# Kernel tuning notes

Hardware: AMD Instinct MI355X
Metric: run time of the kernel (lower is better)

Reference implementation:

```python
import jax, jax.numpy as jnp
import numpy as np

N_INST = 131072      # total patches across all bags
D_EMB = 512          # VGG16 pooling='max' output dim
ATT_UNITS = 128
CLS_UNITS = 512
NUM_BAGS = 256


def setup_inputs() -> dict:
    key = jax.random.key(0)
    ks = jax.random.split(key, 16)
    first_emb = jax.random.normal(ks[0], (N_INST, D_EMB), dtype=jnp.float32)
    first_lab = jnp.sort(jax.random.randint(ks[1], (N_INST,), 0, NUM_BAGS)).astype(jnp.int64)
    s = 0.02
    return {
        "first_emb": first_emb,
        "first_lab": first_lab,
        # first-level attention head: Dense(tanh) -> Dense(1, sigmoid)
        "W_a1": jax.random.normal(ks[2], (D_EMB, ATT_UNITS), dtype=jnp.float32) * s,
        "b_a1": jnp.zeros((ATT_UNITS,), dtype=jnp.float32),
        "w_o1": jax.random.normal(ks[3], (ATT_UNITS, 1), dtype=jnp.float32) * s,
        "b_o1": jnp.zeros((1,), dtype=jnp.float32),
        # second-level attention head
        "W_a2": jax.random.normal(ks[4], (D_EMB, ATT_UNITS), dtype=jnp.float32) * s,
        "b_a2": jnp.zeros((ATT_UNITS,), dtype=jnp.float32),
        "w_o2": jax.random.normal(ks[5], (ATT_UNITS, 1), dtype=jnp.float32) * s,
        "b_o2": jnp.zeros((1,), dtype=jnp.float32),
        # classifier: Dense(CLS_UNITS, linear) -> Dense(1, sigmoid)
        "W_c": jax.random.normal(ks[6], (D_EMB, CLS_UNITS), dtype=jnp.float32) * s,
        "b_c": jnp.zeros((CLS_UNITS,), dtype=jnp.float32),
        "w_out": jax.random.normal(ks[7], (CLS_UNITS, 1), dtype=jnp.float32) * s,
        "b_out": jnp.zeros((1,), dtype=jnp.float32),
    }


def reference(first_emb, first_lab, W_a1, b_a1, w_o1, b_o1,
              W_a2, b_a2, w_o2, b_o2, W_c, b_c, w_out, b_out):
    # --- first-level (instance) attention ---
    a1 = jnp.tanh(first_emb @ W_a1 + b_a1)                 # [N, A]
    att1 = jax.nn.sigmoid(a1 @ w_o1 + b_o1)                # [N, 1]
    # tf: transpose(softmax(transpose(att))) == softmax over the N axis (global)
    fst_att = jax.nn.softmax(att1, axis=0)                 # [N, 1]
    # --- per-bag attention-weighted sum (fused segment reduce) ---
    # replaces the python loop of gather_nd + matmul over contiguous bags
    second_emb = jax.ops.segment_sum(fst_att * first_emb, first_lab,
                                     num_segments=NUM_BAGS)  # [B, D]
    # --- second-level (bag) attention ---
    a2 = jnp.tanh(second_emb @ W_a2 + b_a2)                # [B, A]
    att2 = jax.nn.sigmoid(a2 @ w_o2 + b_o2)                # [B, 1]
    snd_att = jax.nn.softmax(att2.T, axis=-1)              # [1, B]
    outer_bag_emb = snd_att @ second_emb                   # [1, D]
    # --- classifier (dropout is identity at inference) ---
    h = outer_bag_emb @ W_c + b_c                          # [1, CLS]
    pred = jax.nn.sigmoid(h @ w_out + b_out)               # [1, 1]
    return pred
```

## Files before the change

### kernel.cpp

```cpp
#include <hip/hip_runtime.h>
#include <cstdint>
#include <cstddef>

#define N_INST 131072
#define D_EMB  512
#define ATT    128
#define NBAGS  256
#define TILE_I 32
#define LDA    520
#define NBLK   512
#define NTILES (N_INST / TILE_I)
#define TPB    (NTILES / NBLK)
#define NZ1    32

typedef __attribute__((ext_vector_type(8))) short  bf16x8;
typedef __attribute__((ext_vector_type(4))) float  f32x4;
typedef __attribute__((ext_vector_type(4))) unsigned short u16x4;


__device__ inline unsigned short f2b(float f) {
    unsigned u = __builtin_bit_cast(unsigned, f);
    u += 0x7FFFu + ((u >> 16) & 1u);
    return (unsigned short)(u >> 16);
}

__device__ inline float fast_tanh(float x) {
    float e = __expf(2.f * x);
    return 1.f - 2.f / (e + 1.f);
}

__global__ __launch_bounds__(256) void k_prep_wt(
    const float* __restrict__ Wa1, unsigned short* __restrict__ Wt)
{
    const int n = blockIdx.x;
    for (int k = threadIdx.x; k < D_EMB; k += 256)
        Wt[(size_t)n * D_EMB + k] = f2b(Wa1[(size_t)k * ATT + n]);
}

__global__ __launch_bounds__(256, 2) void k_att1(
    const float* __restrict__ emb, const int* __restrict__ lab,
    const unsigned short* __restrict__ Wt, const float* __restrict__ ba1,
    const float* __restrict__ wo1, const float* __restrict__ bo1,
    float* __restrict__ rawr, int R, float* __restrict__ Z1s)
{
    __shared__ unsigned short Ash[2][TILE_I * LDA];
    __shared__ float att4[4][TILE_I];
    __shared__ float sval[TILE_I];
    __shared__ int   labs[2][TILE_I];

    const int t  = threadIdx.x;
    const int w  = t >> 6;
    const int l  = t & 63;
    const int l4 = l & 15;
    const int h4 = l >> 4;
    const int n0 = 16 * (2 * w) + l4;
    const int n1 = 16 * (2 * w + 1) + l4;
    const size_t tile0 = (size_t)blockIdx.x * TPB;
    float* __restrict__ raw = rawr + (size_t)(blockIdx.x % R) * (NBAGS * D_EMB);

    const float ba1v0 = ba1[n0], ba1v1 = ba1[n1];
    const float wo1v0 = wo1[n0], wo1v1 = wo1[n1];

    {
        const size_t i0 = tile0 * TILE_I;
        float4 v[16];
        #pragma unroll
        for (int j = 0; j < 16; ++j) {
            int idx = j * 256 + t;
            int row = idx >> 7;
            int c4  = (idx & 127) * 4;
            v[j] = *reinterpret_cast<const float4*>(&emb[(i0 + row) * D_EMB + c4]);
        }
        if (t < TILE_I) labs[0][t] = lab[i0 + t];
        #pragma unroll
        for (int j = 0; j < 16; ++j) {
            int idx = j * 256 + t;
            int row = idx >> 7;
            int c4  = (idx & 127) * 4;
            u16x4 b = { f2b(v[j].x), f2b(v[j].y), f2b(v[j].z), f2b(v[j].w) };
            *reinterpret_cast<u16x4*>(&Ash[0][row * LDA + c4]) = b;
        }
    }
    __syncthreads();

    int   cur_bag = -1;
    float ar0 = 0.f, ar1 = 0.f;
    float z1acc = 0.f;
    int   p = 0;

    for (int it = 0; it < TPB; ++it) {
        const bool hasNext = (it + 1 < TPB);
        const size_t i0n = (tile0 + it + 1) * TILE_I;

        float4 v[16];
        int nlab = 0;
        if (hasNext) {
            #pragma unroll
            for (int j = 0; j < 16; ++j) {
                int idx = j * 256 + t;
                int row = idx >> 7;
                int c4  = (idx & 127) * 4;
                v[j] = *reinterpret_cast<const float4*>(
                    &emb[(i0n + row) * D_EMB + c4]);
            }
            if (t < TILE_I) nlab = lab[i0n + t];
        }

        f32x4 acc00 = {0.f,0.f,0.f,0.f}, acc01 = {0.f,0.f,0.f,0.f};
        f32x4 acc10 = {0.f,0.f,0.f,0.f}, acc11 = {0.f,0.f,0.f,0.f};
        #pragma unroll
        for (int ks = 0; ks < 16; ++ks) {
            bf16x8 b0 = *reinterpret_cast<const bf16x8*>(
                &Wt[(size_t)n0 * D_EMB + 32 * ks + 8 * h4]);
            bf16x8 b1 = *reinterpret_cast<const bf16x8*>(
                &Wt[(size_t)n1 * D_EMB + 32 * ks + 8 * h4]);
            bf16x8 a0 = *reinterpret_cast<const bf16x8*>(
                &Ash[p][(l4) * LDA + 32 * ks + 8 * h4]);
            bf16x8 a1 = *reinterpret_cast<const bf16x8*>(
                &Ash[p][(16 + l4) * LDA + 32 * ks + 8 * h4]);
            acc00 = __builtin_amdgcn_mfma_f32_16x16x32_bf16(a0, b0, acc00, 0, 0, 0);
            acc01 = __builtin_amdgcn_mfma_f32_16x16x32_bf16(a0, b1, acc01, 0, 0, 0);
            acc10 = __builtin_amdgcn_mfma_f32_16x16x32_bf16(a1, b0, acc10, 0, 0, 0);
            acc11 = __builtin_amdgcn_mfma_f32_16x16x32_bf16(a1, b1, acc11, 0, 0, 0);
        }

        #pragma unroll
        for (int rt = 0; rt < 2; ++rt) {
            #pragma unroll
            for (int reg = 0; reg < 4; ++reg) {
                float pp = fast_tanh((rt ? acc10[reg] : acc00[reg]) + ba1v0) * wo1v0
                         + fast_tanh((rt ? acc11[reg] : acc01[reg]) + ba1v1) * wo1v1;
                pp += __shfl_xor(pp, 1);
                pp += __shfl_xor(pp, 2);
                pp += __shfl_xor(pp, 4);
                pp += __shfl_xor(pp, 8);
                if (l4 == 0) att4[w][16 * rt + 4 * h4 + reg] = pp;
            }
        }

        if (hasNext) {
            #pragma unroll
            for (int j = 0; j < 16; ++j) {
                int idx = j * 256 + t;
                int row = idx >> 7;
                int c4  = (idx & 127) * 4;
                u16x4 b = { f2b(v[j].x), f2b(v[j].y), f2b(v[j].z), f2b(v[j].w) };
                *reinterpret_cast<u16x4*>(&Ash[p ^ 1][row * LDA + c4]) = b;
            }
            if (t < TILE_I) labs[p ^ 1][t] = nlab;
        }
        __syncthreads();

        if (t < TILE_I) {
            float a  = att4[0][t] + att4[1][t] + att4[2][t] + att4[3][t] + bo1[0];
            float sg = 1.f / (1.f + __expf(-a));
            float s  = __expf(sg);
            sval[t]  = s;
            float z = s;
            z += __shfl_xor(z, 1);
            z += __shfl_xor(z, 2);
            z += __shfl_xor(z, 4);
            z += __shfl_xor(z, 8);
            z += __shfl_xor(z, 16);
            if (t == 0) z1acc += z;
        }
        __syncthreads();

        {
            int s0 = 0;
            while (s0 < TILE_I) {
                int bag = labs[p][s0];
                int s1 = s0 + 1;
                while (s1 < TILE_I && labs[p][s1] == bag) ++s1;
                if (bag != cur_bag) {
                    if (cur_bag >= 0) {
                        atomicAdd(&raw[cur_bag * D_EMB + 2 * t], ar0);
                        atomicAdd(&raw[cur_bag * D_EMB + 2 * t + 1], ar1);
                    }
                    ar0 = 0.f; ar1 = 0.f; cur_bag = bag;
                }
                for (int ii = s0; ii < s1; ++ii) {
                    unsigned u = *reinterpret_cast<const unsigned*>(
                        &Ash[p][(size_t)ii * LDA + 2 * t]);
                    float lo = __builtin_bit_cast(float, u << 16);
                    float hi = __builtin_bit_cast(float, u & 0xffff0000u);
                    float s  = sval[ii];
                    ar0 = fmaf(s, lo, ar0);
                    ar1 = fmaf(s, hi, ar1);
                }
                s0 = s1;
            }
        }
        __syncthreads();
        p ^= 1;
    }

    if (cur_bag >= 0) {
        atomicAdd(&raw[cur_bag * D_EMB + 2 * t], ar0);
        atomicAdd(&raw[cur_bag * D_EMB + 2 * t + 1], ar1);
    }
    if (t == 0) atomicAdd(&Z1s[blockIdx.x & (NZ1 - 1)], z1acc);
}

__global__ __launch_bounds__(128) void k_att2(
    const float* __restrict__ Wa2, const float* __restrict__ ba2,
    const float* __restrict__ wo2, const float* __restrict__ bo2,
    float* __restrict__ rawr, int R, const float* __restrict__ Z1s,
    float* __restrict__ e2, float* __restrict__ Z2)
{
    __shared__ float sec[D_EMB];
    __shared__ float hh[2];
    const int b = blockIdx.x;
    const int t = threadIdx.x;
    float zsum = 0.f;
    #pragma unroll
    for (int i = 0; i < NZ1; ++i) zsum += Z1s[i];
    const float zinv = 1.f / zsum;
    for (int d = t; d < D_EMB; d += 128) {
        float s = 0.f;
        for (int r = 0; r < R; ++r)
            s += rawr[(size_t)r * (NBAGS * D_EMB) + b * D_EMB + d];
        float v = s * zinv;
        rawr[b * D_EMB + d] = v;
        sec[d] = v;
    }
    __syncthreads();
    float dot = 0.f;
    #pragma unroll 8
    for (int d = 0; d < D_EMB; ++d) dot = fmaf(sec[d], Wa2[d * ATT + t], dot);
    float h = fast_tanh(dot + ba2[t]) * wo2[t];
    #pragma unroll
    for (int m = 1; m < 64; m <<= 1) h += __shfl_xor(h, m);
    if ((t & 63) == 0) hh[t >> 6] = h;
    __syncthreads();
    if (t == 0) {
        float a  = hh[0] + hh[1] + bo2[0];
        float sg = 1.f / (1.f + __expf(-a));
        float e  = __expf(sg);
        e2[b] = e;
        atomicAdd(Z2, e);
    }
}

__global__ __launch_bounds__(256) void k_v(
    const float* __restrict__ Wc, const float* __restrict__ wout,
    float* __restrict__ v)
{
    const int t   = threadIdx.x;
    const int row = blockIdx.x * 8 + (t >> 5);
    const int l   = t & 31;
    float s = 0.f;
    #pragma unroll 4
    for (int c = l; c < 512; c += 32) s = fmaf(Wc[(size_t)row * 512 + c], wout[c], s);
    #pragma unroll
    for (int m = 1; m < 32; m <<= 1) s += __shfl_xor(s, m);
    if (l == 0) v[row] = s;
}

__global__ __launch_bounds__(256) void k_pool(
    const float* __restrict__ raw, const float* __restrict__ e2,
    float* __restrict__ outer)
{
    const int t  = threadIdx.x;
    const int b0 = blockIdx.x * 32;
    float o0 = 0.f, o1 = 0.f;
    for (int b = b0; b < b0 + 32; ++b) {
        float wgt = e2[b];
        float2 r = *reinterpret_cast<const float2*>(&raw[b * D_EMB + 2 * t]);
        o0 = fmaf(wgt, r.x, o0);
        o1 = fmaf(wgt, r.y, o1);
    }
    atomicAdd(&outer[2 * t], o0);
    atomicAdd(&outer[2 * t + 1], o1);
}

__global__ __launch_bounds__(256) void k_cls(
    const float* __restrict__ outer, const float* __restrict__ Z2,
    const float* __restrict__ v, const float* __restrict__ bc,
    const float* __restrict__ wout, const float* __restrict__ bout,
    float* __restrict__ out)
{
    __shared__ float pp[4];
    const int t = threadIdx.x;
    const float z2inv = 1.f / Z2[0];
    float p = (outer[2 * t] * v[2 * t] + outer[2 * t + 1] * v[2 * t + 1]) * z2inv
            + bc[2 * t] * wout[2 * t] + bc[2 * t + 1] * wout[2 * t + 1];
    #pragma unroll
    for (int m = 1; m < 64; m <<= 1) p += __shfl_xor(p, m);
    if ((t & 63) == 0) pp[t >> 6] = p;
    __syncthreads();
    if (t == 0) {
        float s = pp[0] + pp[1] + pp[2] + pp[3] + bout[0];
        out[0] = 1.f / (1.f + __expf(-s));
    }
}

extern "C" void kernel_launch(void* const* d_in, const int* in_sizes, int n_in,
                              void* d_out, int out_size, void* d_ws, size_t ws_size,
                              hipStream_t stream)
{
    const float* emb  = (const float*)d_in[0];
    const int*   lab  = (const int*)d_in[1];
    const float* Wa1  = (const float*)d_in[2];
    const float* ba1  = (const float*)d_in[3];
    const float* wo1  = (const float*)d_in[4];
    const float* bo1  = (const float*)d_in[5];
    const float* Wa2  = (const float*)d_in[6];
    const float* ba2  = (const float*)d_in[7];
    const float* wo2  = (const float*)d_in[8];
    const float* bo2  = (const float*)d_in[9];
    const float* Wc   = (const float*)d_in[10];
    const float* bc   = (const float*)d_in[11];
    const float* wout = (const float*)d_in[12];
    const float* bout = (const float*)d_in[13];

    float* ws    = (float*)d_ws;
    float* Z1s   = ws + 0;
    float* Z2    = ws + 32;
    float* v     = ws + 64;
    float* e2    = ws + 1024;
    float* outer = ws + 1536;
    unsigned short* Wt = (unsigned short*)(ws + 4096);
    float* rawr  = ws + 36864;

    const size_t need8 = ((size_t)36864 + 8u * NBAGS * D_EMB) * sizeof(float);
    const int R = (ws_size >= need8) ? 8 : 1;

    hipMemsetAsync(d_ws, 0, ((size_t)36864 + (size_t)R * NBAGS * D_EMB) * sizeof(float), stream);

    hipLaunchKernelGGL(k_prep_wt, dim3(ATT),   dim3(256), 0, stream, Wa1, Wt);
    hipLaunchKernelGGL(k_v,       dim3(64),    dim3(256), 0, stream, Wc, wout, v);
    hipLaunchKernelGGL(k_att1,    dim3(NBLK),  dim3(256), 0, stream,
                       emb, lab, Wt, ba1, wo1, bo1, rawr, R, Z1s);
    hipLaunchKernelGGL(k_att2,    dim3(NBAGS), dim3(128), 0, stream,
                       Wa2, ba2, wo2, bo2, rawr, R, Z1s, e2, Z2);
    hipLaunchKernelGGL(k_pool,    dim3(8),     dim3(256), 0, stream,
                       rawr, e2, outer);
    hipLaunchKernelGGL(k_cls,     dim3(1),     dim3(256), 0, stream,
                       outer, Z2, v, bc, wout, bout, (float*)d_out);
}
```

Before: 139.9 us.

## Keep fp32 tiles in registers and do segment sum from registers

Restructures the att1 loop so each thread keeps the current and next fp32 tile in registers (ping-pong via a two-step unrolled lambda). The bf16 conversion to LDS happens at the start of each step, which drops the shared label array and its scan loop. The per-bag weighted sum now reads the fp32 register copies directly, with bag ids and weights broadcast by shuffles, and each thread handles two rows per tile across 4 columns. This removes LDS re-reads and the serial run-length scan, and sums from fp32 rather than bf16 data. The cost is doubled register pressure (32 float4s), which may lower occupancy below the launch bound of 2 blocks per CU.

```diff
diff --git a/kernel.cpp b/kernel.cpp
--- a/kernel.cpp
+++ b/kernel.cpp
@@ -46,7 +46,6 @@
     __shared__ unsigned short Ash[2][TILE_I * LDA];
     __shared__ float att4[4][TILE_I];
     __shared__ float sval[TILE_I];
-    __shared__ int   labs[2][TILE_I];
 
     const int t  = threadIdx.x;
     const int w  = t >> 6;
@@ -55,56 +54,48 @@
     const int h4 = l >> 4;
     const int n0 = 16 * (2 * w) + l4;
     const int n1 = 16 * (2 * w + 1) + l4;
+    const int c  = t & 127;
+    const int hf = t >> 7;
     const size_t tile0 = (size_t)blockIdx.x * TPB;
     float* __restrict__ raw = rawr + (size_t)(blockIdx.x % R) * (NBAGS * D_EMB);
 
     const float ba1v0 = ba1[n0], ba1v1 = ba1[n1];
     const float wo1v0 = wo1[n0], wo1v1 = wo1[n1];
 
+    float4 vA[16], vB[16];
+    int lvA = 0, lvB = 0;
+
     {
         const size_t i0 = tile0 * TILE_I;
-        float4 v[16];
-        #pragma unroll
-        for (int j = 0; j < 16; ++j) {
-            int idx = j * 256 + t;
-            int row = idx >> 7;
-            int c4  = (idx & 127) * 4;
-            v[j] = *reinterpret_cast<const float4*>(&emb[(i0 + row) * D_EMB + c4]);
-        }
-        if (t < TILE_I) labs[0][t] = lab[i0 + t];
-        #pragma unroll
-        for (int j = 0; j < 16; ++j) {
-            int idx = j * 256 + t;
-            int row = idx >> 7;
-            int c4  = (idx & 127) * 4;
-            u16x4 b = { f2b(v[j].x), f2b(v[j].y), f2b(v[j].z), f2b(v[j].w) };
-            *reinterpret_cast<u16x4*>(&Ash[0][row * LDA + c4]) = b;
-        }
-    }
-    __syncthreads();
+        #pragma unroll
+        for (int j = 0; j < 16; ++j)
+            vA[j] = *reinterpret_cast<const float4*>(
+                &emb[(i0 + 2 * j + hf) * D_EMB + 4 * c]);
+        lvA = lab[i0 + (l & 31)];
+    }
 
     int   cur_bag = -1;
-    float ar0 = 0.f, ar1 = 0.f;
+    float ar0 = 0.f, ar1 = 0.f, ar2 = 0.f, ar3 = 0.f;
     float z1acc = 0.f;
-    int   p = 0;
-
-    for (int it = 0; it < TPB; ++it) {
+
+    auto step = [&](float4 (&vC)[16], float4 (&vN)[16], int lvC, int &lvN,
+                    int p, int it) {
         const bool hasNext = (it + 1 < TPB);
         const size_t i0n = (tile0 + it + 1) * TILE_I;
 
-        float4 v[16];
-        int nlab = 0;
+        #pragma unroll
+        for (int j = 0; j < 16; ++j) {
+            u16x4 b = { f2b(vC[j].x), f2b(vC[j].y), f2b(vC[j].z), f2b(vC[j].w) };
+            *reinterpret_cast<u16x4*>(&Ash[p][(2 * j + hf) * LDA + 4 * c]) = b;
+        }
         if (hasNext) {
             #pragma unroll
-            for (int j = 0; j < 16; ++j) {
-                int idx = j * 256 + t;
-                int row = idx >> 7;
-                int c4  = (idx & 127) * 4;
-                v[j] = *reinterpret_cast<const float4*>(
-                    &emb[(i0n + row) * D_EMB + c4]);
-            }
-            if (t < TILE_I) nlab = lab[i0n + t];
-        }
+            for (int j = 0; j < 16; ++j)
+                vN[j] = *reinterpret_cast<const float4*>(
+                    &emb[(i0n + 2 * j + hf) * D_EMB + 4 * c]);
+            lvN = lab[i0n + (l & 31)];
+        }
+        __syncthreads();
 
         f32x4 acc00 = {0.f,0.f,0.f,0.f}, acc01 = {0.f,0.f,0.f,0.f};
         f32x4 acc10 = {0.f,0.f,0.f,0.f}, acc11 = {0.f,0.f,0.f,0.f};
@@ -137,18 +128,6 @@
                 if (l4 == 0) att4[w][16 * rt + 4 * h4 + reg] = pp;
             }
         }
-
-        if (hasNext) {
-            #pragma unroll
-            for (int j = 0; j < 16; ++j) {
-                int idx = j * 256 + t;
-                int row = idx >> 7;
-                int c4  = (idx & 127) * 4;
-                u16x4 b = { f2b(v[j].x), f2b(v[j].y), f2b(v[j].z), f2b(v[j].w) };
-                *reinterpret_cast<u16x4*>(&Ash[p ^ 1][row * LDA + c4]) = b;
-            }
-            if (t < TILE_I) labs[p ^ 1][t] = nlab;
-        }
         __syncthreads();
 
         if (t < TILE_I) {
@@ -166,38 +145,38 @@
         }
         __syncthreads();
 
-        {
-            int s0 = 0;
-            while (s0 < TILE_I) {
-                int bag = labs[p][s0];
-                int s1 = s0 + 1;
-                while (s1 < TILE_I && labs[p][s1] == bag) ++s1;
-                if (bag != cur_bag) {
-                    if (cur_bag >= 0) {
-                        atomicAdd(&raw[cur_bag * D_EMB + 2 * t], ar0);
-                        atomicAdd(&raw[cur_bag * D_EMB + 2 * t + 1], ar1);
-                    }
-                    ar0 = 0.f; ar1 = 0.f; cur_bag = bag;
+        float s_reg = sval[l & 31];
+        #pragma unroll
+        for (int j = 0; j < 16; ++j) {
+            const int r = 2 * j + hf;
+            int   bag = __shfl(lvC, r);
+            float s   = __shfl(s_reg, r);
+            if (bag != cur_bag) {
+                if (cur_bag >= 0) {
+                    float* dst = &raw[cur_bag * D_EMB + 4 * c];
+                    atomicAdd(dst + 0, ar0); atomicAdd(dst + 1, ar1);
+                    atomicAdd(dst + 2, ar2); atomicAdd(dst + 3, ar3);
                 }
-                for (int ii = s0; ii < s1; ++ii) {
-                    unsigned u = *reinterpret_cast<const unsigned*>(
-                        &Ash[p][(size_t)ii * LDA + 2 * t]);
-                    float lo = __builtin_bit_cast(float, u << 16);
-                    float hi = __builtin_bit_cast(float, u & 0xffff0000u);
-                    float s  = sval[ii];
-                    ar0 = fmaf(s, lo, ar0);
-                    ar1 = fmaf(s, hi, ar1);
-                }
-                s0 = s1;
+                ar0 = ar1 = ar2 = ar3 = 0.f;
+                cur_bag = bag;
             }
-        }
-        __syncthreads();
-        p ^= 1;
+            ar0 = fmaf(s, vC[j].x, ar0);
+            ar1 = fmaf(s, vC[j].y, ar1);
+            ar2 = fmaf(s, vC[j].z, ar2);
+            ar3 = fmaf(s, vC[j].w, ar3);
+        }
+    };
+
+    #pragma unroll
+    for (int it = 0; it < TPB; it += 2) {
+        step(vA, vB, lvA, lvB, 0, it);
+        step(vB, vA, lvB, lvA, 1, it + 1);
     }
 
     if (cur_bag >= 0) {
-        atomicAdd(&raw[cur_bag * D_EMB + 2 * t], ar0);
-        atomicAdd(&raw[cur_bag * D_EMB + 2 * t + 1], ar1);
+        float* dst = &raw[cur_bag * D_EMB + 4 * c];
+        atomicAdd(dst + 0, ar0); atomicAdd(dst + 1, ar1);
+        atomicAdd(dst + 2, ar2); atomicAdd(dst + 3, ar3);
     }
     if (t == 0) atomicAdd(&Z1s[blockIdx.x & (NZ1 - 1)], z1acc);
 }
```

Result: slower. 185.8 us (+32.8%).
